# Optimization experiments

Hardware: AMD Instinct MI355X
Metric: run time of the kernel (lower is better)

## Reference

```python
import jax, jax.numpy as jnp
import numpy as np

B, S, N, M, D = 1, 8, 768, 768, 64
K, RATIO, IT, THR = 8, 0.6, 16, 0.75
R_N, R_M = int(RATIO * N), int(RATIO * M)


def _solver(sx, sy, sm):
    # mask-weighted cross-correlation model: (Bi, D, D)
    w = sm.astype(sx.dtype)
    num = jnp.einsum('bnd,bnm,bme->bde', sx, w, sy)
    den = jnp.sum(w, axis=(-2, -1))[:, None, None] + 1e-6
    return num / den


def _evaluator(models, x, y, mask):
    # squared L2 residual ||x @ model - y||^2, NaN where mask is False -> (Bi, N, M)
    xt = jnp.einsum('bnd,bde->bne', x, models)
    sq = (jnp.sum(xt * xt, -1)[:, :, None] + jnp.sum(y * y, -1)[:, None, :]
          - 2.0 * jnp.einsum('bne,bme->bnm', xt, y))
    return jnp.where(mask, sq, jnp.nan)


def _ransac(x, y, mask, perm1, perm2):
    Bi, n, d = x.shape
    m = y.shape[1]
    p1 = perm1.reshape(-1)  # (IT*R_N,) values in [0, R_N)
    p2 = perm2.reshape(-1)
    s_x = x[:, p1].reshape(Bi * IT, R_N, d)
    s_y = y[:, p2].reshape(Bi * IT, R_M, d)
    s_m = mask[:, p1].reshape(Bi, IT, R_N, m)
    s_m = jnp.take_along_axis(s_m, perm2[None, :, None, :], axis=-1)
    s_m = s_m.reshape(Bi * IT, R_N, R_M)
    models = _solver(s_x, s_y, s_m)  # (Bi*IT, D, D)
    xr = jnp.broadcast_to(x[:, None], (Bi, IT, n, d)).reshape(Bi * IT, n, d)
    yr = jnp.broadcast_to(y[:, None], (Bi, IT, m, d)).reshape(Bi * IT, m, d)
    mr = jnp.broadcast_to(mask[:, None], (Bi, IT, n, m)).reshape(Bi * IT, n, m)
    errors = _evaluator(models, xr, yr, mr).reshape(Bi, IT, n, m)
    models = models.reshape(Bi, IT, D, D)
    avg = jnp.nanmean(errors, axis=(-1, -2))  # (Bi, IT)
    best = jnp.argmin(avg, axis=-1)
    best_model = jnp.take_along_axis(models, best[:, None, None, None], axis=1)[:, 0]
    best_errors = jnp.take_along_axis(errors, best[:, None, None, None], axis=1)[:, 0]
    thrs = jnp.nanquantile(best_errors, THR, axis=-1, keepdims=True)
    inliers = best_errors < thrs
    return best_model, inliers, best_errors


def _forward(qk, kks, qmask, kmask, perm1, perm2):
    mask = qmask & kmask  # (B*S, N, M)
    x = jnp.broadcast_to(qk[:, None], (B, S, N, D)).reshape(B * S, N, D)
    y = kks.reshape(B * S, M, D)
    bm, inl, be = _ransac(x, y, mask, perm1, perm2)
    bm = bm.reshape(B, S, D, D)
    inl = inl.reshape(B, S, N, M)
    be = be.reshape(B, S, N, M)
    avg = jnp.nanmean(be, axis=(-2, -1))  # (B, S)
    topk_err, topk_idx = jax.lax.top_k(avg, K)  # torch.topk default: largest
    tm = jnp.take_along_axis(bm, topk_idx[:, :, None, None], axis=1)
    ti = jnp.take_along_axis(inl, topk_idx[:, :, None, None], axis=1)
    return ti, tm, topk_err


def setup_inputs() -> dict:
    key = jax.random.key(0)
    k1, k2, k3, k4, k5, k6 = jax.random.split(key, 6)
    qk = jax.random.normal(k1, (B, N, D), jnp.float32)
    kks = jax.random.normal(k2, (B, S, M, D), jnp.float32)
    qmask = jax.random.randint(k3, (B * S, N, M), 0, 2) > 0
    kmask = jax.random.randint(k4, (B * S, N, M), 0, 2) > 0
    # _batch_randperm: permutations of [0, r_n)
    perm1 = jnp.argsort(jax.random.uniform(k5, (IT, R_N)), axis=-1).astype(jnp.int32)
    perm2 = jnp.argsort(jax.random.uniform(k6, (IT, R_M)), axis=-1).astype(jnp.int32)
    return {"qk": qk, "kks": kks, "qmask": qmask, "kmask": kmask,
            "perm1": perm1, "perm2": perm2}


def reference(qk, kks, qmask, kmask, perm1, perm2):
    return _forward(qk, kks, qmask, kmask, perm1, perm2)
```

## Files before the change

kernel.cpp:

```cpp
#include <hip/hip_runtime.h>
#include <math.h>

#define NN 768
#define MM 768
#define DD 64
#define BI 8
#define RN 460
#define KTOP 8

static constexpr size_t OFF_TI = 0;
static constexpr size_t OFF_TM = (size_t)KTOP * NN * MM;
static constexpr size_t OFF_TE = OFF_TM + (size_t)KTOP * DD * DD;

static constexpr size_t TP_OFF    = 0;
static constexpr size_t NUMP_OFF  = TP_OFF + (size_t)8 * BI * RN * DD;
static constexpr size_t MODEL_OFF = NUMP_OFF + (size_t)32 * BI * DD * DD;
static constexpr size_t XT_OFF    = MODEL_OFF + (size_t)BI * DD * DD;
static constexpr size_t ERR_OFF   = XT_OFF + (size_t)BI * NN * DD;
static constexpr size_t FEND      = ERR_OFF + (size_t)BI * NN * MM;
static constexpr size_t ESUM_B = FEND * 4;
static constexpr size_t ECNT_B = ESUM_B + 1152 * 4;
static constexpr size_t DENP_B = ECNT_B + 1152 * 4;
static constexpr size_t PM_B   = DENP_B + 512 * 4 + 32;

__device__ __forceinline__ unsigned f2key(float f) {
  unsigned u = __float_as_uint(f);
  return (u & 0x80000000u) ? ~u : (u | 0x80000000u);
}
__device__ __forceinline__ float key2f(unsigned k) {
  unsigned u = (k & 0x80000000u) ? (k ^ 0x80000000u) : ~k;
  return __uint_as_float(u);
}

__global__ __launch_bounds__(256) void k_pack(
    const void* __restrict__ qm, const void* __restrict__ km,
    unsigned long long* __restrict__ pmw) {
  __shared__ __align__(16) unsigned char nib[768];
  __shared__ int flg[4];
  const int tid = threadIdx.x, lane = tid & 63, g = tid >> 6;
  {
    unsigned w0 = ((const unsigned*)qm)[tid];
    unsigned long long any = __ballot((w0 & 0xFFFFFF00u) != 0);
    if (lane == 0) flg[g] = (any != 0) ? 1 : 0;
  }
  __syncthreads();
  const int flag = (flg[0] | flg[1] | flg[2] | flg[3]) ? 0 : 1;
  const int rg = blockIdx.x, b = blockIdx.y;
  const size_t E0 = ((size_t)b * NN + (size_t)rg * 4) * MM;
  unsigned nb[3];
#pragma unroll
  for (int k = 0; k < 3; k++) {
    int gi = tid + 256 * k;
    size_t e = E0 + 4 * (size_t)gi;
    unsigned nibble;
    if (flag) {
      uint4 qa = *(const uint4*)((const int*)qm + e);
      uint4 ka = *(const uint4*)((const int*)km + e);
      nibble = ((qa.x && ka.x) ? 1u : 0u) | ((qa.y && ka.y) ? 2u : 0u) |
               ((qa.z && ka.z) ? 4u : 0u) | ((qa.w && ka.w) ? 8u : 0u);
    } else {
      unsigned qa = *(const unsigned*)((const unsigned char*)qm + e);
      unsigned ka = *(const unsigned*)((const unsigned char*)km + e);
      nibble = (((qa & 0xFFu) && (ka & 0xFFu)) ? 1u : 0u) |
               (((qa & 0xFF00u) && (ka & 0xFF00u)) ? 2u : 0u) |
               (((qa & 0xFF0000u) && (ka & 0xFF0000u)) ? 4u : 0u) |
               (((qa & 0xFF000000u) && (ka & 0xFF000000u)) ? 8u : 0u);
    }
    nb[k] = nibble;
  }
#pragma unroll
  for (int k = 0; k < 3; k++) nib[tid + 256 * k] = (unsigned char)nb[k];
  __syncthreads();
  if (tid < 48) {
    uint4 q4 = *(const uint4*)&nib[tid * 16];
    unsigned long long w = 0;
    unsigned dw[4] = {q4.x, q4.y, q4.z, q4.w};
#pragma unroll
    for (int q = 0; q < 4; q++) {
      w |= (unsigned long long)(dw[q] & 0xFu) << (16 * q + 0);
      w |= (unsigned long long)((dw[q] >> 8) & 0xFu) << (16 * q + 4);
      w |= (unsigned long long)((dw[q] >> 16) & 0xFu) << (16 * q + 8);
      w |= (unsigned long long)((dw[q] >> 24) & 0xFu) << (16 * q + 12);
    }
    int n = rg * 4 + tid / 12, ww = tid % 12;
    pmw[((size_t)b * NN + n) * 12 + ww] = w;
  }
}

__global__ __launch_bounds__(256) void k_tgemm(
    const float* __restrict__ kks, const unsigned long long* __restrict__ pmw,
    float* __restrict__ tpart, int* __restrict__ denp) {
  __shared__ float ys[64 * 68];
  __shared__ int cntsh[4];
  const int tid = threadIdx.x, lane = tid & 63, g = tid >> 6;
  const int ntile = blockIdx.x, c = blockIdx.y, b = blockIdx.z;
  const int m0 = c * 64;
  const float* yb = kks + (size_t)b * MM * DD;
  for (int q = tid; q < 1024; q += 256) {
    int r = q >> 4, col = (q & 15) * 4;
    *(float4*)&ys[r * 68 + col] = *(const float4*)&yb[(size_t)(m0 + r) * DD + col];
  }
  const int n0 = ntile * 64 + g * 16;
  unsigned wlo[16], whi[16];
  int cnt = 0;
#pragma unroll
  for (int i = 0; i < 16; i++) {
    int n = n0 + i;
    unsigned long long w = pmw[((size_t)b * NN + n) * 12 + c];
    if (c == 7) w &= 0xFFFULL;
    wlo[i] = (unsigned)w; whi[i] = (unsigned)(w >> 32);
    if (n < RN) cnt += __builtin_popcountll(w);
  }
  __syncthreads();
  float acc[16];
#pragma unroll
  for (int i = 0; i < 16; i++) acc[i] = 0.f;
#pragma unroll 4
  for (int m = 0; m < 32; m++) {
    int yi = __float_as_int(ys[m * 68 + lane]);
#pragma unroll
    for (int i = 0; i < 16; i++) {
      int sel = ((int)(wlo[i] << (31 - m))) >> 31;
      acc[i] += __int_as_float(yi & sel);
    }
  }
#pragma unroll 4
  for (int m = 0; m < 32; m++) {
    int yi = __float_as_int(ys[(m + 32) * 68 + lane]);
#pragma unroll
    for (int i = 0; i < 16; i++) {
      int sel = ((int)(whi[i] << (31 - m))) >> 31;
      acc[i] += __int_as_float(yi & sel);
    }
  }
#pragma unroll
  for (int i = 0; i < 16; i++) {
    int n = n0 + i;
    if (n < RN)
      tpart[(((size_t)c * BI + b) * RN + n) * DD + lane] = acc[i];
  }
  if (lane == 0) cntsh[g] = cnt;
  __syncthreads();
  if (tid == 0) denp[(b * 8 + c) * 8 + ntile] = cntsh[0] + cntsh[1] + cntsh[2] + cntsh[3];
}

__global__ __launch_bounds__(256) void k_num(
    const float* __restrict__ qk, const float* __restrict__ tpart, float* __restrict__ numpart) {
  __shared__ float xs[16 * 64];
  __shared__ float ts[16 * 64];
  const int tid = threadIdx.x, lane = tid & 63, g = tid >> 6;
  const int chunk = blockIdx.x, b = blockIdx.y;
  for (int l = tid; l < 1024; l += 256) {
    int r = l >> 6, col = l & 63;
    int n = chunk * 16 + r;
    float xv = 0.f, tv = 0.f;
    if (n < RN) {
      xv = qk[(size_t)n * DD + col];
#pragma unroll
      for (int cc = 0; cc < 8; cc++)
        tv += tpart[(((size_t)cc * BI + b) * RN + n) * DD + col];
    }
    xs[l] = xv; ts[l] = tv;
  }
  __syncthreads();
  float acc[16];
#pragma unroll
  for (int i = 0; i < 16; i++) acc[i] = 0.f;
#pragma unroll 4
  for (int r = 0; r < 16; r++) {
    float tv = ts[r * 64 + lane];
#pragma unroll
    for (int i = 0; i < 16; i++) acc[i] += xs[r * 64 + g + i * 4] * tv;
  }
#pragma unroll
  for (int i = 0; i < 16; i++)
    numpart[((size_t)chunk * BI + b) * (DD * DD) + (size_t)(g + i * 4) * DD + lane] = acc[i];
}

__global__ __launch_bounds__(256) void k_model(
    const float* __restrict__ numpart, const int* __restrict__ denp, float* __restrict__ model) {
  __shared__ float invp;
  const int tid = threadIdx.x;
  const int b = blockIdx.x >> 3, part = blockIdx.x & 7;
  if (tid < 64) {
    int v = denp[b * 64 + tid];
#pragma unroll
    for (int o = 32; o > 0; o >>= 1) v += __shfl_xor(v, o);
    if (tid == 0) invp = 1.f / ((float)v + 1e-6f);
  }
  __syncthreads();
  float inv = invp;
  for (int l = part * 512 + tid; l < part * 512 + 512; l += 256) {
    float s = 0.f;
#pragma unroll
    for (int cc = 0; cc < 32; cc++) s += numpart[((size_t)cc * BI + b) * (DD * DD) + l];
    model[(size_t)b * (DD * DD) + l] = s * inv;
  }
}

__global__ __launch_bounds__(256) void k_xt(
    const float* __restrict__ qk, const float* __restrict__ model, float* __restrict__ xt) {
  __shared__ float ml[DD * DD];
  const int tid = threadIdx.x, lane = tid & 63, g = tid >> 6;
  const int seg = blockIdx.x, b = blockIdx.y;
  const float4* msrc = (const float4*)(model + (size_t)b * DD * DD);
  for (int q = tid; q < 1024; q += 256) ((float4*)ml)[q] = msrc[q];
  __syncthreads();
#pragma unroll
  for (int rr = 0; rr < 6; rr++) {
    int n = seg * 24 + g * 6 + rr;
    float acc = 0.f;
#pragma unroll 8
    for (int d = 0; d < DD; d++) acc += qk[(size_t)n * DD + d] * ml[d * DD + lane];
    xt[((size_t)b * NN + n) * DD + lane] = acc;
  }
}

__global__ __launch_bounds__(256) void k_err(
    const float* __restrict__ xt, const float* __restrict__ kks,
    const unsigned long long* __restrict__ pmw,
    float* __restrict__ err, float* __restrict__ esum, int* __restrict__ ecnt) {
  __shared__ float As[64 * 68];
  __shared__ float Bs[64 * 68];
  __shared__ float xx[64], yy[64];
  __shared__ float rsum[256];
  __shared__ int rcnt[256];
  const int b = blockIdx.z, wj = blockIdx.x;
  const int i0 = blockIdx.y * 64, j0 = wj * 64;
  const int tid = threadIdx.x, tx = tid & 15, ty = tid >> 4;
  const float* xb = xt + ((size_t)b * NN + i0) * DD;
  const float* yb = kks + ((size_t)b * MM + j0) * DD;
  for (int q = tid; q < 1024; q += 256) {
    int r = q >> 4, c = q & 15;
    *(float4*)&As[r * 68 + c * 4] = ((const float4*)(xb + (size_t)r * DD))[c];
    *(float4*)&Bs[r * 68 + c * 4] = ((const float4*)(yb + (size_t)r * DD))[c];
  }
  __syncthreads();
  if (tid < 64) {
    float s = 0.f;
#pragma unroll 8
    for (int k2 = 0; k2 < 64; k2++) { float v = As[tid * 68 + k2]; s += v * v; }
    xx[tid] = s;
  } else if (tid < 128) {
    int r = tid - 64;
    float s = 0.f;
#pragma unroll 8
    for (int k2 = 0; k2 < 64; k2++) { float v = Bs[r * 68 + k2]; s += v * v; }
    yy[r] = s;
  }
  __syncthreads();
  float acc[4][4];
#pragma unroll
  for (int ii = 0; ii < 4; ii++)
#pragma unroll
    for (int jj = 0; jj < 4; jj++) acc[ii][jj] = 0.f;
  for (int k2 = 0; k2 < 64; k2 += 4) {
    float4 av[4], bv[4];
#pragma unroll
    for (int ii = 0; ii < 4; ii++) av[ii] = *(const float4*)&As[(ty + 16 * ii) * 68 + k2];
#pragma unroll
    for (int jj = 0; jj < 4; jj++) bv[jj] = *(const float4*)&Bs[(tx + 16 * jj) * 68 + k2];
#pragma unroll
    for (int ii = 0; ii < 4; ii++)
#pragma unroll
      for (int jj = 0; jj < 4; jj++)
        acc[ii][jj] += av[ii].x * bv[jj].x + av[ii].y * bv[jj].y +
                       av[ii].z * bv[jj].z + av[ii].w * bv[jj].w;
  }
  float psum = 0.f;
  int pcnt = 0;
#pragma unroll
  for (int ii = 0; ii < 4; ii++) {
    int i = i0 + ty + 16 * ii;
    unsigned long long word = pmw[((size_t)b * NN + i) * 12 + wj];
    size_t rowb = ((size_t)b * NN + i) * MM;
#pragma unroll
    for (int jj = 0; jj < 4; jj++) {
      int j = j0 + tx + 16 * jj;
      int cm = (int)((word >> (tx + 16 * jj)) & 1ULL);
      float v = xx[ty + 16 * ii] + yy[tx + 16 * jj] - 2.f * acc[ii][jj];
      if (cm) { err[rowb + j] = v; psum += v; pcnt++; }
    }
  }
  rsum[tid] = psum;
  rcnt[tid] = pcnt;
  __syncthreads();
  for (int s = 128; s > 0; s >>= 1) {
    if (tid < s) { rsum[tid] += rsum[tid + s]; rcnt[tid] += rcnt[tid + s]; }
    __syncthreads();
  }
  if (tid == 0) {
    int t = b * 144 + blockIdx.y * 12 + wj;
    esum[t] = rsum[0];
    ecnt[t] = rcnt[0];
  }
}

__global__ __launch_bounds__(256) void k_quant(
    const float* __restrict__ err, const unsigned long long* __restrict__ pmw,
    const float* __restrict__ esum, const int* __restrict__ ecnt,
    const float* __restrict__ model, float* __restrict__ out) {
  __shared__ float avg_sh[BI];
  __shared__ int ords_sh[BI];
  const int bid = blockIdx.x, tid = threadIdx.x, lane = tid & 63, g = tid >> 6;
  const float INF = __builtin_inff();
  for (int h = 0; h < 2; h++) {
    int b = g * 2 + h, base = b * 144;
    float s = esum[base + lane] + esum[base + 64 + lane] + ((lane < 16) ? esum[base + 128 + lane] : 0.f);
    int ct = ecnt[base + lane] + ecnt[base + 64 + lane] + ((lane < 16) ? ecnt[base + 128 + lane] : 0);
#pragma unroll
    for (int o = 32; o > 0; o >>= 1) { s += __shfl_xor(s, o); ct += __shfl_xor(ct, o); }
    if (lane == 0) avg_sh[b] = s / (float)ct;
  }
  __syncthreads();
  if (tid == 0) {
    unsigned used = 0;
#pragma unroll
    for (int k = 0; k < KTOP; k++) {
      int best = 0;
      float bv = -INF;
#pragma unroll
      for (int b = 0; b < BI; b++)
        if (!((used >> b) & 1u) && avg_sh[b] > bv) { bv = avg_sh[b]; best = b; }
      used |= 1u << best;
      ords_sh[k] = best;
    }
  }
  __syncthreads();
  if (bid == 0) {
    if (tid < KTOP) out[OFF_TE + tid] = avg_sh[ords_sh[tid]];
    for (int l = tid; l < KTOP * DD * DD; l += 256) {
      int k = l >> 12;
      out[OFF_TM + l] = model[(size_t)ords_sh[k] * (DD * DD) + (l & (DD * DD - 1))];
    }
  }
  const int kk = bid >> 6, seg = bid & 63;
  const int b = ords_sh[kk];
  for (int rr = 0; rr < 3; rr++) {
    int n = seg * 12 + g * 3 + rr;
    const float* row = err + ((size_t)b * NN + n) * MM;
    size_t prow = ((size_t)b * NN + n) * 12;
    unsigned long long wd[3];
#pragma unroll
    for (int w = 0; w < 3; w++) wd[w] = pmw[prow + w * 4 + (lane >> 4)];
    int cp = (lane < 12) ? __builtin_popcountll(pmw[prow + lane]) : 0;
#pragma unroll
    for (int o = 32; o > 0; o >>= 1) cp += __shfl_xor(cp, o);
    const int cnt = cp;
    float v[12];
#pragma unroll
    for (int w = 0; w < 3; w++) {
      float4 f4 = ((const float4*)row)[w * 64 + lane];
      v[w * 4 + 0] = f4.x; v[w * 4 + 1] = f4.y; v[w * 4 + 2] = f4.z; v[w * 4 + 3] = f4.w;
    }
    unsigned key[12];
    unsigned mnk = 0xFFFFFFFFu, mxk = 0u;
#pragma unroll
    for (int r = 0; r < 12; r++) {
      int bit = (int)((wd[r >> 2] >> (((lane & 15) << 2) + (r & 3))) & 1ULL);
      unsigned kf = f2key(v[r]);
      key[r] = bit ? kf : 0xFFFFFFFFu;
      mnk = min(mnk, key[r]);
      mxk = max(mxk, bit ? kf : 0u);
    }
#pragma unroll
    for (int o = 32; o > 0; o >>= 1) {
      mnk = min(mnk, (unsigned)__shfl_xor((int)mnk, o));
      mxk = max(mxk, (unsigned)__shfl_xor((int)mxk, o));
    }
    float thr;
    if (cnt == 0) {
      thr = -INF;
    } else {
      float pos = 0.75f * (float)(cnt - 1);
      int k0 = (int)pos;
      float f = pos - (float)k0;
      int target = k0 + 1;
      unsigned lo = mnk, hi = mxk;
      while (lo < hi) {
        unsigned mid = lo + ((hi - lo) >> 1);
        int c = 0;
#pragma unroll
        for (int r = 0; r < 12; r++) c += __builtin_popcountll(__ballot(key[r] <= mid));
        if (c >= target) hi = mid; else lo = mid + 1;
      }
      unsigned ka = lo;
      float a = key2f(ka);
      float b2;
      if (k0 + 1 >= cnt) {
        b2 = a;
      } else {
        int c1 = 0;
#pragma unroll
        for (int r = 0; r < 12; r++) c1 += __builtin_popcountll(__ballot(key[r] <= ka));
        if (c1 >= k0 + 2) {
          b2 = a;
        } else {
          unsigned mn = 0xFFFFFFFFu;
#pragma unroll
          for (int r = 0; r < 12; r++) mn = min(mn, (key[r] > ka) ? key[r] : 0xFFFFFFFFu);
#pragma unroll
          for (int o = 32; o > 0; o >>= 1) mn = min(mn, (unsigned)__shfl_xor((int)mn, o));
          b2 = key2f(mn);
        }
      }
      thr = a + f * (b2 - a);
    }
    float* orow = out + OFF_TI + ((size_t)kk * NN + n) * MM;
#pragma unroll
    for (int w = 0; w < 3; w++) {
      unsigned long long ww = wd[w];
      int sh = (lane & 15) << 2;
      float4 o;
      o.x = (((ww >> (sh + 0)) & 1ULL) && v[w * 4 + 0] < thr) ? 1.f : 0.f;
      o.y = (((ww >> (sh + 1)) & 1ULL) && v[w * 4 + 1] < thr) ? 1.f : 0.f;
      o.z = (((ww >> (sh + 2)) & 1ULL) && v[w * 4 + 2] < thr) ? 1.f : 0.f;
      o.w = (((ww >> (sh + 3)) & 1ULL) && v[w * 4 + 3] < thr) ? 1.f : 0.f;
      ((float4*)orow)[w * 64 + lane] = o;
    }
  }
}

extern "C" void kernel_launch(void* const* d_in, const int* in_sizes, int n_in,
                              void* d_out, int out_size, void* d_ws, size_t ws_size,
                              hipStream_t stream) {
  (void)in_sizes; (void)n_in; (void)out_size; (void)ws_size;
  const float* qk  = (const float*)d_in[0];
  const float* kks = (const float*)d_in[1];
  const void*  qm  = d_in[2];
  const void*  km  = d_in[3];
  float* out = (float*)d_out;
  float* wsf = (float*)d_ws;
  char*  wsb = (char*)d_ws;
  float* tpart   = wsf + TP_OFF;
  float* numpart = wsf + NUMP_OFF;
  float* model   = wsf + MODEL_OFF;
  float* xtb     = wsf + XT_OFF;
  float* errb    = wsf + ERR_OFF;
  float* esum = (float*)(wsb + ESUM_B);
  int*   ecnt = (int*)(wsb + ECNT_B);
  int*   denp = (int*)(wsb + DENP_B);
  unsigned long long* pmw = (unsigned long long*)(wsb + PM_B);

  k_pack<<<dim3(192, BI), 256, 0, stream>>>(qm, km, pmw);
  k_tgemm<<<dim3(8, 8, BI), 256, 0, stream>>>(kks, pmw, tpart, denp);
  k_num<<<dim3(32, BI), 256, 0, stream>>>(qk, tpart, numpart);
  k_model<<<64, 256, 0, stream>>>(numpart, denp, model);
  k_xt<<<dim3(32, BI), 256, 0, stream>>>(qk, model, xtb);
  k_err<<<dim3(12, 12, BI), 256, 0, stream>>>(xtb, kks, pmw, errb, esum, ecnt);
  k_quant<<<512, 256, 0, stream>>>(errb, pmw, esum, ecnt, model, out);
}
```

Before: 178.4 us.

## Fuse mask packing, masked Y-sum and X^T·T product into one solver kernel

Result: slower. 194.3 us (+8.9%).

```diff
diff --git a/kernel.cpp b/kernel.cpp
--- a/kernel.cpp
+++ b/kernel.cpp
@@ -12,9 +12,8 @@
 static constexpr size_t OFF_TM = (size_t)KTOP * NN * MM;
 static constexpr size_t OFF_TE = OFF_TM + (size_t)KTOP * DD * DD;
 
-static constexpr size_t TP_OFF    = 0;
-static constexpr size_t NUMP_OFF  = TP_OFF + (size_t)8 * BI * RN * DD;
-static constexpr size_t MODEL_OFF = NUMP_OFF + (size_t)32 * BI * DD * DD;
+static constexpr size_t NUMP_OFF  = 0;
+static constexpr size_t MODEL_OFF = NUMP_OFF + (size_t)64 * BI * DD * DD;
 static constexpr size_t XT_OFF    = MODEL_OFF + (size_t)BI * DD * DD;
 static constexpr size_t ERR_OFF   = XT_OFF + (size_t)BI * NN * DD;
 static constexpr size_t FEND      = ERR_OFF + (size_t)BI * NN * MM;
@@ -32,12 +31,52 @@
   return __uint_as_float(u);
 }
 
-__global__ __launch_bounds__(256) void k_pack(
+__device__ __forceinline__ unsigned pack4(const void* qm, const void* km, int flag, size_t e) {
+  if (flag) {
+    uint4 qa = *(const uint4*)((const unsigned*)qm + e);
+    uint4 ka = *(const uint4*)((const unsigned*)km + e);
+    return ((qa.x && ka.x) ? 1u : 0u) | ((qa.y && ka.y) ? 2u : 0u) |
+           ((qa.z && ka.z) ? 4u : 0u) | ((qa.w && ka.w) ? 8u : 0u);
+  } else {
+    unsigned qa = *(const unsigned*)((const unsigned char*)qm + e);
+    unsigned ka = *(const unsigned*)((const unsigned char*)km + e);
+    return (((qa & 0xFFu) && (ka & 0xFFu)) ? 1u : 0u) |
+           (((qa & 0xFF00u) && (ka & 0xFF00u)) ? 2u : 0u) |
+           (((qa & 0xFF0000u) && (ka & 0xFF0000u)) ? 4u : 0u) |
+           (((qa & 0xFF000000u) && (ka & 0xFF000000u)) ? 8u : 0u);
+  }
+}
+
+__device__ __forceinline__ unsigned long long asm16(uint4 q4) {
+  unsigned dw[4] = {q4.x, q4.y, q4.z, q4.w};
+  unsigned long long w = 0;
+#pragma unroll
+  for (int q = 0; q < 4; q++) {
+    w |= (unsigned long long)(dw[q] & 0xFu) << (16 * q + 0);
+    w |= (unsigned long long)((dw[q] >> 8) & 0xFu) << (16 * q + 4);
+    w |= (unsigned long long)((dw[q] >> 16) & 0xFu) << (16 * q + 8);
+    w |= (unsigned long long)((dw[q] >> 24) & 0xFu) << (16 * q + 12);
+  }
+  return w;
+}
+
+__global__ __launch_bounds__(256) void k_solve(
+    const float* __restrict__ qk, const float* __restrict__ kks,
     const void* __restrict__ qm, const void* __restrict__ km,
+    float* __restrict__ numpart, int* __restrict__ denp,
     unsigned long long* __restrict__ pmw) {
-  __shared__ __align__(16) unsigned char nib[768];
+  __shared__ float ys[64 * 68];
+  __shared__ float xs[64 * 68];
+  __shared__ unsigned char nib[1024];
+  __shared__ unsigned char nib2[1280];
+  __shared__ unsigned long long words[64];
+  __shared__ int cntsh[4];
   __shared__ int flg[4];
   const int tid = threadIdx.x, lane = tid & 63, g = tid >> 6;
+  const int ntile = blockIdx.x, c = blockIdx.y, b = blockIdx.z;
+  const int n0 = ntile * 64, m0 = c * 64;
+  const int blin = c * 8 + ntile;
+
   {
     unsigned w0 = ((const unsigned*)qm)[tid];
     unsigned long long any = __ballot((w0 & 0xFFFFFF00u) != 0);
@@ -45,73 +84,62 @@
   }
   __syncthreads();
   const int flag = (flg[0] | flg[1] | flg[2] | flg[3]) ? 0 : 1;
-  const int rg = blockIdx.x, b = blockIdx.y;
-  const size_t E0 = ((size_t)b * NN + (size_t)rg * 4) * MM;
-  unsigned nb[3];
-#pragma unroll
-  for (int k = 0; k < 3; k++) {
+
+  unsigned nbA[4];
+#pragma unroll
+  for (int k = 0; k < 4; k++) {
     int gi = tid + 256 * k;
-    size_t e = E0 + 4 * (size_t)gi;
-    unsigned nibble;
-    if (flag) {
-      uint4 qa = *(const uint4*)((const int*)qm + e);
-      uint4 ka = *(const uint4*)((const int*)km + e);
-      nibble = ((qa.x && ka.x) ? 1u : 0u) | ((qa.y && ka.y) ? 2u : 0u) |
-               ((qa.z && ka.z) ? 4u : 0u) | ((qa.w && ka.w) ? 8u : 0u);
-    } else {
-      unsigned qa = *(const unsigned*)((const unsigned char*)qm + e);
-      unsigned ka = *(const unsigned*)((const unsigned char*)km + e);
-      nibble = (((qa & 0xFFu) && (ka & 0xFFu)) ? 1u : 0u) |
-               (((qa & 0xFF00u) && (ka & 0xFF00u)) ? 2u : 0u) |
-               (((qa & 0xFF0000u) && (ka & 0xFF0000u)) ? 4u : 0u) |
-               (((qa & 0xFF000000u) && (ka & 0xFF000000u)) ? 8u : 0u);
-    }
-    nb[k] = nibble;
-  }
-#pragma unroll
-  for (int k = 0; k < 3; k++) nib[tid + 256 * k] = (unsigned char)nb[k];
-  __syncthreads();
-  if (tid < 48) {
-    uint4 q4 = *(const uint4*)&nib[tid * 16];
-    unsigned long long w = 0;
-    unsigned dw[4] = {q4.x, q4.y, q4.z, q4.w};
-#pragma unroll
-    for (int q = 0; q < 4; q++) {
-      w |= (unsigned long long)(dw[q] & 0xFu) << (16 * q + 0);
-      w |= (unsigned long long)((dw[q] >> 8) & 0xFu) << (16 * q + 4);
-      w |= (unsigned long long)((dw[q] >> 16) & 0xFu) << (16 * q + 8);
-      w |= (unsigned long long)((dw[q] >> 24) & 0xFu) << (16 * q + 12);
-    }
-    int n = rg * 4 + tid / 12, ww = tid % 12;
-    pmw[((size_t)b * NN + n) * 12 + ww] = w;
-  }
-}
-
-__global__ __launch_bounds__(256) void k_tgemm(
-    const float* __restrict__ kks, const unsigned long long* __restrict__ pmw,
-    float* __restrict__ tpart, int* __restrict__ denp) {
-  __shared__ float ys[64 * 68];
-  __shared__ int cntsh[4];
-  const int tid = threadIdx.x, lane = tid & 63, g = tid >> 6;
-  const int ntile = blockIdx.x, c = blockIdx.y, b = blockIdx.z;
-  const int m0 = c * 64;
-  const float* yb = kks + (size_t)b * MM * DD;
+    int r = gi >> 4, cc = (gi & 15) * 4;
+    size_t e = ((size_t)b * NN + n0 + r) * MM + m0 + cc;
+    nbA[k] = pack4(qm, km, flag, e);
+  }
+  unsigned nbB[5];
+#pragma unroll
+  for (int k = 0; k < 5; k++) {
+    int t = tid + 256 * k;
+    int wi = t >> 4, q4i = t & 15;
+    int W = blin * 80 + wi;
+    int n, w;
+    if (W < 3072) { n = 512 + W / 12; w = W % 12; }
+    else          { int r = W - 3072; n = r >> 2; w = 8 + (r & 3); }
+    size_t e = ((size_t)b * NN + n) * MM + (size_t)w * 64 + q4i * 4;
+    nbB[k] = pack4(qm, km, flag, e);
+  }
   for (int q = tid; q < 1024; q += 256) {
     int r = q >> 4, col = (q & 15) * 4;
-    *(float4*)&ys[r * 68 + col] = *(const float4*)&yb[(size_t)(m0 + r) * DD + col];
-  }
-  const int n0 = ntile * 64 + g * 16;
+    *(float4*)&ys[r * 68 + col] = *(const float4*)&kks[((size_t)b * MM + m0 + r) * DD + col];
+    *(float4*)&xs[r * 68 + col] = *(const float4*)&qk[(size_t)(n0 + r) * DD + col];
+  }
+#pragma unroll
+  for (int k = 0; k < 4; k++) nib[tid + 256 * k] = (unsigned char)nbA[k];
+#pragma unroll
+  for (int k = 0; k < 5; k++) nib2[tid + 256 * k] = (unsigned char)nbB[k];
+  __syncthreads();
+  if (tid < 64) {
+    unsigned long long w = asm16(*(const uint4*)&nib[tid * 16]);
+    words[tid] = w;
+    pmw[((size_t)b * NN + n0 + tid) * 12 + c] = w;
+  } else if (tid >= 128 && tid < 208) {
+    int wi = tid - 128;
+    unsigned long long w = asm16(*(const uint4*)&nib2[wi * 16]);
+    int W = blin * 80 + wi;
+    int n, ww;
+    if (W < 3072) { n = 512 + W / 12; ww = W % 12; }
+    else          { int r = W - 3072; n = r >> 2; ww = 8 + (r & 3); }
+    pmw[((size_t)b * NN + n) * 12 + ww] = w;
+  }
+  __syncthreads();
+
   unsigned wlo[16], whi[16];
   int cnt = 0;
 #pragma unroll
   for (int i = 0; i < 16; i++) {
-    int n = n0 + i;
-    unsigned long long w = pmw[((size_t)b * NN + n) * 12 + c];
+    int nl = g * 16 + i;
+    unsigned long long w = words[nl];
     if (c == 7) w &= 0xFFFULL;
     wlo[i] = (unsigned)w; whi[i] = (unsigned)(w >> 32);
-    if (n < RN) cnt += __builtin_popcountll(w);
-  }
-  __syncthreads();
+    if (n0 + nl < RN) cnt += __builtin_popcountll(w);
+  }
   float acc[16];
 #pragma unroll
   for (int i = 0; i < 16; i++) acc[i] = 0.f;
@@ -133,48 +161,29 @@
       acc[i] += __int_as_float(yi & sel);
     }
   }
+  if (lane == 0) cntsh[g] = cnt;
+  __syncthreads();
+  if (tid == 0) denp[blin * 8 + b] = cntsh[0] + cntsh[1] + cntsh[2] + cntsh[3];
+
+  float* tl = ys;
 #pragma unroll
   for (int i = 0; i < 16; i++) {
-    int n = n0 + i;
-    if (n < RN)
-      tpart[(((size_t)c * BI + b) * RN + n) * DD + lane] = acc[i];
-  }
-  if (lane == 0) cntsh[g] = cnt;
-  __syncthreads();
-  if (tid == 0) denp[(b * 8 + c) * 8 + ntile] = cntsh[0] + cntsh[1] + cntsh[2] + cntsh[3];
-}
-
-__global__ __launch_bounds__(256) void k_num(
-    const float* __restrict__ qk, const float* __restrict__ tpart, float* __restrict__ numpart) {
-  __shared__ float xs[16 * 64];
-  __shared__ float ts[16 * 64];
-  const int tid = threadIdx.x, lane = tid & 63, g = tid >> 6;
-  const int chunk = blockIdx.x, b = blockIdx.y;
-  for (int l = tid; l < 1024; l += 256) {
-    int r = l >> 6, col = l & 63;
-    int n = chunk * 16 + r;
-    float xv = 0.f, tv = 0.f;
-    if (n < RN) {
-      xv = qk[(size_t)n * DD + col];
-#pragma unroll
-      for (int cc = 0; cc < 8; cc++)
-        tv += tpart[(((size_t)cc * BI + b) * RN + n) * DD + col];
-    }
-    xs[l] = xv; ts[l] = tv;
-  }
-  __syncthreads();
-  float acc[16];
-#pragma unroll
-  for (int i = 0; i < 16; i++) acc[i] = 0.f;
+    int nl = g * 16 + i;
+    tl[nl * 68 + lane] = (n0 + nl < RN) ? acc[i] : 0.f;
+  }
+  __syncthreads();
+  float acc2[16];
+#pragma unroll
+  for (int i = 0; i < 16; i++) acc2[i] = 0.f;
 #pragma unroll 4
-  for (int r = 0; r < 16; r++) {
-    float tv = ts[r * 64 + lane];
-#pragma unroll
-    for (int i = 0; i < 16; i++) acc[i] += xs[r * 64 + g + i * 4] * tv;
-  }
-#pragma unroll
-  for (int i = 0; i < 16; i++)
-    numpart[((size_t)chunk * BI + b) * (DD * DD) + (size_t)(g + i * 4) * DD + lane] = acc[i];
+  for (int n = 0; n < 64; n++) {
+    float tv = tl[n * 68 + lane];
+#pragma unroll
+    for (int i = 0; i < 16; i++) acc2[i] += xs[n * 68 + (g + 4 * i)] * tv;
+  }
+  float* np = numpart + ((size_t)blin * BI + b) * (DD * DD);
+#pragma unroll
+  for (int i = 0; i < 16; i++) np[(size_t)(g + 4 * i) * DD + lane] = acc2[i];
 }
 
 __global__ __launch_bounds__(256) void k_model(
@@ -183,7 +192,7 @@
   const int tid = threadIdx.x;
   const int b = blockIdx.x >> 3, part = blockIdx.x & 7;
   if (tid < 64) {
-    int v = denp[b * 64 + tid];
+    int v = denp[tid * 8 + b];
 #pragma unroll
     for (int o = 32; o > 0; o >>= 1) v += __shfl_xor(v, o);
     if (tid == 0) invp = 1.f / ((float)v + 1e-6f);
@@ -193,7 +202,7 @@
   for (int l = part * 512 + tid; l < part * 512 + 512; l += 256) {
     float s = 0.f;
 #pragma unroll
-    for (int cc = 0; cc < 32; cc++) s += numpart[((size_t)cc * BI + b) * (DD * DD) + l];
+    for (int bl = 0; bl < 64; bl++) s += numpart[((size_t)bl * BI + b) * (DD * DD) + l];
     model[(size_t)b * (DD * DD) + l] = s * inv;
   }
 }
@@ -432,7 +441,6 @@
   float* out = (float*)d_out;
   float* wsf = (float*)d_ws;
   char*  wsb = (char*)d_ws;
-  float* tpart   = wsf + TP_OFF;
   float* numpart = wsf + NUMP_OFF;
   float* model   = wsf + MODEL_OFF;
   float* xtb     = wsf + XT_OFF;
@@ -442,9 +450,7 @@
   int*   denp = (int*)(wsb + DENP_B);
   unsigned long long* pmw = (unsigned long long*)(wsb + PM_B);
 
-  k_pack<<<dim3(192, BI), 256, 0, stream>>>(qm, km, pmw);
-  k_tgemm<<<dim3(8, 8, BI), 256, 0, stream>>>(kks, pmw, tpart, denp);
-  k_num<<<dim3(32, BI), 256, 0, stream>>>(qk, tpart, numpart);
+  k_solve<<<dim3(8, 8, BI), 256, 0, stream>>>(qk, kks, qm, km, numpart, denp, pmw);
   k_model<<<64, 256, 0, stream>>>(numpart, denp, model);
   k_xt<<<dim3(32, BI), 256, 0, stream>>>(qk, model, xtb);
   k_err<<<dim3(12, 12, BI), 256, 0, stream>>>(xtb, kks, pmw, errb, esum, ecnt);
```
